# Performance work log

Measured on AMD Instinct MI355X. Metric: run time of the kernel, lower is better.

Reference implementation:

```python
import jax, jax.numpy as jnp
import numpy as np

N, F_IN, F_OUT = 8192, 512, 256

def setup_inputs() -> dict:
    key = jax.random.key(0)
    kx, kW, ka = jax.random.split(key, 3)
    x = jax.random.normal(kx, (N, F_IN), dtype=jnp.float32)
    adj = jnp.ones((N, N), dtype=jnp.float32)  # accepted but unused by the original forward
    # nn.Linear(in, out, bias=False) stores weight as [out, in]
    W = jax.random.normal(kW, (F_OUT, F_IN), dtype=jnp.float32) * 0.02
    # nn.Linear(2*out, 1, bias=False) -> attention vector of length 2*F_OUT
    a = jax.random.normal(ka, (2 * F_OUT,), dtype=jnp.float32) * 0.02
    return {"x": x, "adj": adj, "W": W, "a": a}

def reference(x, adj, W, a):
    # h = W(x): [N, F_OUT]
    h = x @ W.T
    # Original concatenates [h_i, h_j] for all pairs (O(N^2 * 2F) memory) and
    # applies linear a. Since a is linear, e_ij = a1.h_i + a2.h_j -> broadcast add.
    a_src, a_dst = a[:F_OUT], a[F_OUT:]
    e = (h @ a_src)[:, None] + (h @ a_dst)[None, :]  # [N, N]
    attention = jax.nn.softmax(e, axis=1)             # row-wise over neighbors j
    h_prime = attention @ h                           # [N, F_OUT]
    return h_prime
```

## Files before the change

### kernel.cpp

```cpp
#include <hip/hip_runtime.h>
#include <math.h>

#define NN 8192
#define FIN 512
#define FOUT 256
#define FBLK 512
#define NU 8


__global__ __launch_bounds__(256) void compute_g(const float* __restrict__ W,
                                                 const float* __restrict__ a_dst,
                                                 float* __restrict__ g,
                                                 float* __restrict__ u8,
                                                 float* __restrict__ S) {
    __shared__ float red[4][64];
    const int tid = threadIdx.x;

    const int zi = blockIdx.x * 256 + tid;
    ((float2*)u8)[zi] = make_float2(0.f, 0.f);
    if (zi == 0) *S = 0.f;

    const int kl = tid & 63;
    const int cp = tid >> 6;
    const int k = blockIdx.x * 64 + kl;
    float s = 0.f;
    #pragma unroll 8
    for (int c = cp * 64; c < cp * 64 + 64; ++c)
        s = fmaf(W[(size_t)c * FIN + k], a_dst[c], s);
    red[cp][kl] = s;
    __syncthreads();
    if (cp == 0) g[k] = red[0][kl] + red[1][kl] + red[2][kl] + red[3][kl];
}

__global__ __launch_bounds__(256) void fused_pass(const float* __restrict__ x,
                                                  const float* __restrict__ g,
                                                  float* __restrict__ u8,
                                                  float* __restrict__ S) {
    __shared__ float us[4][FIN];
    __shared__ float sred[4];
    const int tid = threadIdx.x;
    const int lane = tid & 63;
    const int wave = tid >> 6;
    const int r0 = blockIdx.x * 16;

    const float4* g4 = (const float4*)g;
    const float4 g0 = g4[lane], g1 = g4[lane + 64];

    float4 xa[4], xb[4];
    float w[4];
    #pragma unroll
    for (int rr = 0; rr < 4; ++rr) {
        const float4* xr = (const float4*)(x + (size_t)(r0 + wave * 4 + rr) * FIN);
        xa[rr] = xr[lane];
        xb[rr] = xr[lane + 64];
        float s = xa[rr].x * g0.x + xa[rr].y * g0.y + xa[rr].z * g0.z + xa[rr].w * g0.w
                + xb[rr].x * g1.x + xb[rr].y * g1.y + xb[rr].z * g1.z + xb[rr].w * g1.w;
        #pragma unroll
        for (int off = 32; off; off >>= 1) s += __shfl_xor(s, off);
        w[rr] = __expf(s);
    }
    if (lane == 0) sred[wave] = w[0] + w[1] + w[2] + w[3];

    float4 pa = make_float4(0.f, 0.f, 0.f, 0.f);
    float4 pb = make_float4(0.f, 0.f, 0.f, 0.f);
    #pragma unroll
    for (int rr = 0; rr < 4; ++rr) {
        pa.x = fmaf(w[rr], xa[rr].x, pa.x); pa.y = fmaf(w[rr], xa[rr].y, pa.y);
        pa.z = fmaf(w[rr], xa[rr].z, pa.z); pa.w = fmaf(w[rr], xa[rr].w, pa.w);
        pb.x = fmaf(w[rr], xb[rr].x, pb.x); pb.y = fmaf(w[rr], xb[rr].y, pb.y);
        pb.z = fmaf(w[rr], xb[rr].z, pb.z); pb.w = fmaf(w[rr], xb[rr].w, pb.w);
    }
    ((float4*)&us[wave][0])[lane] = pa;
    ((float4*)&us[wave][FOUT])[lane] = pb;
    __syncthreads();

    float* ub = u8 + (size_t)(blockIdx.x & (NU - 1)) * FIN;
    float v0 = us[0][tid] + us[1][tid] + us[2][tid] + us[3][tid];
    float v1 = us[0][tid + 256] + us[1][tid + 256] + us[2][tid + 256] + us[3][tid + 256];
    atomicAdd(&ub[tid], v0);
    atomicAdd(&ub[tid + 256], v1);
    if (tid == 0) atomicAdd(S, sred[0] + sred[1] + sred[2] + sred[3]);
}

__global__ __launch_bounds__(256) void compute_v(const float* __restrict__ W,
                                                 const float* __restrict__ u8,
                                                 const float* __restrict__ S,
                                                 float* __restrict__ vs) {
    __shared__ float us[FIN];
    const int tid = threadIdx.x;
    float a0 = 0.f, a1 = 0.f;
    #pragma unroll
    for (int i = 0; i < NU; ++i) {
        a0 += u8[(size_t)i * FIN + tid];
        a1 += u8[(size_t)i * FIN + tid + 256];
    }
    us[tid] = a0;
    us[tid + 256] = a1;
    __syncthreads();

    const int lane = tid & 63;
    const int wave = tid >> 6;
    const int c = blockIdx.x * 4 + wave;
    const float4* wr = (const float4*)(W + (size_t)c * FIN);
    const float4* uv = (const float4*)us;
    float4 w0 = wr[lane], w1 = wr[lane + 64];
    float4 u0 = uv[lane], u1 = uv[lane + 64];
    float s = w0.x * u0.x + w0.y * u0.y + w0.z * u0.z + w0.w * u0.w
            + w1.x * u1.x + w1.y * u1.y + w1.z * u1.z + w1.w * u1.w;
    #pragma unroll
    for (int off = 32; off; off >>= 1) s += __shfl_xor(s, off);
    if (lane == 0) vs[c] = s / *S;
}

__global__ __launch_bounds__(256) void broadcast_out(const float* __restrict__ vs,
                                                     float* __restrict__ out) {
    const int idx = blockIdx.x * 256 + threadIdx.x;
    float4 vv = ((const float4*)vs)[idx & 63];
    ((float4*)out)[idx] = vv;
}

extern "C" void kernel_launch(void* const* d_in, const int* in_sizes, int n_in,
                              void* d_out, int out_size, void* d_ws, size_t ws_size,
                              hipStream_t stream) {
    const float* x = (const float*)d_in[0];
    const float* W = (const float*)d_in[2];
    const float* a = (const float*)d_in[3];
    float* out = (float*)d_out;

    float* ws = (float*)d_ws;
    float* g  = ws;
    float* u8 = ws + 512;
    float* S  = ws + 512 + NU * FIN;
    float* vs = S + 16;

    compute_g<<<8, 256, 0, stream>>>(W, a + FOUT, g, u8, S);
    fused_pass<<<FBLK, 256, 0, stream>>>(x, g, u8, S);
    compute_v<<<FOUT / 4, 256, 0, stream>>>(W, u8, S, vs);
    broadcast_out<<<(NN * FOUT / 4) / 256, 256, 0, stream>>>(vs, out);
}
```

Before: 323.3 us.

## Fuse all GAT stages into one cooperative kernel with grid-wide syncs

Replaces the four separate launches with one cooperative kernel that uses grid syncs between stages: computing g, the weighted row reduction into u8 and S, the W·u projection, and the output broadcast. Each block now recomputes the full 256-output projection from W and writes its own 16 output rows directly. This removes per-launch overhead and inter-kernel gaps. In exchange it adds redundant reads of W across all blocks (strided per-thread row access) and the cost of grid barriers. The old four-kernel path remains as a fallback if the cooperative launch fails.

Measured after the change: 463.4 us. 43.3% more time.

```diff
diff --git a/kernel.cpp b/kernel.cpp
--- a/kernel.cpp
+++ b/kernel.cpp
@@ -1,12 +1,131 @@
 #include <hip/hip_runtime.h>
+#include <hip/hip_cooperative_groups.h>
 #include <math.h>
+
+namespace cg = cooperative_groups;
 
 #define NN 8192
 #define FIN 512
 #define FOUT 256
-#define FBLK 512
+#define GRID 512
 #define NU 8
 
+
+__global__ __launch_bounds__(256, 2) void gat_fused_all(
+    const float* __restrict__ x,
+    const float* __restrict__ W,
+    const float* __restrict__ a_dst,
+    float* __restrict__ out,
+    float* __restrict__ g,
+    float* __restrict__ u8,
+    float* __restrict__ S)
+{
+    cg::grid_group gg = cg::this_grid();
+
+    __shared__ float us[4][FIN];
+    __shared__ float sred[4];
+    __shared__ float vsh[FOUT];
+
+    const int tid  = threadIdx.x;
+    const int bid  = blockIdx.x;
+    const int lane = tid & 63;
+    const int wave = tid >> 6;
+    const int r0   = bid * 16;
+
+    if (bid < 8) {
+        const int zi = bid * 256 + tid;
+        ((float2*)u8)[zi] = make_float2(0.f, 0.f);
+        if (zi == 0) *S = 0.f;
+
+        const int k = bid * 64 + lane;
+        float s = 0.f;
+        #pragma unroll 8
+        for (int c = wave * 64; c < wave * 64 + 64; ++c)
+            s = fmaf(W[(size_t)c * FIN + k], a_dst[c], s);
+        us[wave][lane] = s;
+        __syncthreads();
+        if (wave == 0) g[k] = us[0][lane] + us[1][lane] + us[2][lane] + us[3][lane];
+    }
+    gg.sync();
+
+    const float4* g4 = (const float4*)g;
+    const float4 g0 = g4[lane], g1 = g4[lane + 64];
+
+    float4 xa[4], xb[4];
+    float w[4];
+    #pragma unroll
+    for (int rr = 0; rr < 4; ++rr) {
+        const float4* xr = (const float4*)(x + (size_t)(r0 + wave * 4 + rr) * FIN);
+        xa[rr] = xr[lane];
+        xb[rr] = xr[lane + 64];
+        float s = xa[rr].x * g0.x + xa[rr].y * g0.y + xa[rr].z * g0.z + xa[rr].w * g0.w
+                + xb[rr].x * g1.x + xb[rr].y * g1.y + xb[rr].z * g1.z + xb[rr].w * g1.w;
+        #pragma unroll
+        for (int off = 32; off; off >>= 1) s += __shfl_xor(s, off);
+        w[rr] = __expf(s);
+    }
+    if (lane == 0) sred[wave] = w[0] + w[1] + w[2] + w[3];
+
+    float4 pa = make_float4(0.f, 0.f, 0.f, 0.f);
+    float4 pb = make_float4(0.f, 0.f, 0.f, 0.f);
+    #pragma unroll
+    for (int rr = 0; rr < 4; ++rr) {
+        pa.x = fmaf(w[rr], xa[rr].x, pa.x); pa.y = fmaf(w[rr], xa[rr].y, pa.y);
+        pa.z = fmaf(w[rr], xa[rr].z, pa.z); pa.w = fmaf(w[rr], xa[rr].w, pa.w);
+        pb.x = fmaf(w[rr], xb[rr].x, pb.x); pb.y = fmaf(w[rr], xb[rr].y, pb.y);
+        pb.z = fmaf(w[rr], xb[rr].z, pb.z); pb.w = fmaf(w[rr], xb[rr].w, pb.w);
+    }
+    ((float4*)&us[wave][0])[lane]    = pa;
+    ((float4*)&us[wave][FOUT])[lane] = pb;
+    __syncthreads();
+
+    {
+        float* ub = u8 + (size_t)(bid & (NU - 1)) * FIN;
+        float v0 = us[0][tid]       + us[1][tid]       + us[2][tid]       + us[3][tid];
+        float v1 = us[0][tid + 256] + us[1][tid + 256] + us[2][tid + 256] + us[3][tid + 256];
+        atomicAdd(&ub[tid], v0);
+        atomicAdd(&ub[tid + 256], v1);
+        if (tid == 0) atomicAdd(S, sred[0] + sred[1] + sred[2] + sred[3]);
+    }
+    gg.sync();
+
+    {
+        float a0 = 0.f, a1 = 0.f;
+        #pragma unroll
+        for (int i = 0; i < NU; ++i) {
+            a0 += u8[(size_t)i * FIN + tid];
+            a1 += u8[(size_t)i * FIN + tid + 256];
+        }
+        us[0][tid]       = a0;
+        us[0][tid + 256] = a1;
+    }
+    __syncthreads();
+
+    {
+        const float rS = 1.f / (*S);
+        const float4* u4 = (const float4*)&us[0][0];
+        const float4* wr = (const float4*)(W + (size_t)tid * FIN);
+        float s = 0.f;
+        #pragma unroll 16
+        for (int i = 0; i < FIN / 4; ++i) {
+            const float4 wv = wr[i];
+            const float4 uv = u4[i];
+            s += wv.x * uv.x + wv.y * uv.y + wv.z * uv.z + wv.w * uv.w;
+        }
+        vsh[tid] = s * rS;
+    }
+    __syncthreads();
+
+    {
+        const float4* v4 = (const float4*)vsh;
+        float4* ob = (float4*)out + (size_t)r0 * (FOUT / 4);
+        #pragma unroll
+        for (int q = 0; q < 4; ++q) {
+            const int fi = q * 256 + tid;
+            ob[fi] = v4[fi & 63];
+        }
+    }
+}
 
 __global__ __launch_bounds__(256) void compute_g(const float* __restrict__ W,
                                                  const float* __restrict__ a_dst,
@@ -15,11 +134,9 @@
                                                  float* __restrict__ S) {
     __shared__ float red[4][64];
     const int tid = threadIdx.x;
-
     const int zi = blockIdx.x * 256 + tid;
     ((float2*)u8)[zi] = make_float2(0.f, 0.f);
     if (zi == 0) *S = 0.f;
-
     const int kl = tid & 63;
     const int cp = tid >> 6;
     const int k = blockIdx.x * 64 + kl;
@@ -42,10 +159,8 @@
     const int lane = tid & 63;
     const int wave = tid >> 6;
     const int r0 = blockIdx.x * 16;
-
     const float4* g4 = (const float4*)g;
     const float4 g0 = g4[lane], g1 = g4[lane + 64];
-
     float4 xa[4], xb[4];
     float w[4];
     #pragma unroll
@@ -60,7 +175,6 @@
         w[rr] = __expf(s);
     }
     if (lane == 0) sred[wave] = w[0] + w[1] + w[2] + w[3];
-
     float4 pa = make_float4(0.f, 0.f, 0.f, 0.f);
     float4 pb = make_float4(0.f, 0.f, 0.f, 0.f);
     #pragma unroll
@@ -73,7 +187,6 @@
     ((float4*)&us[wave][0])[lane] = pa;
     ((float4*)&us[wave][FOUT])[lane] = pb;
     __syncthreads();
-
     float* ub = u8 + (size_t)(blockIdx.x & (NU - 1)) * FIN;
     float v0 = us[0][tid] + us[1][tid] + us[2][tid] + us[3][tid];
     float v1 = us[0][tid + 256] + us[1][tid + 256] + us[2][tid + 256] + us[3][tid + 256];
@@ -97,7 +210,6 @@
     us[tid] = a0;
     us[tid + 256] = a1;
     __syncthreads();
-
     const int lane = tid & 63;
     const int wave = tid >> 6;
     const int c = blockIdx.x * 4 + wave;
@@ -125,6 +237,7 @@
     const float* x = (const float*)d_in[0];
     const float* W = (const float*)d_in[2];
     const float* a = (const float*)d_in[3];
+    const float* a_dst = a + FOUT;
     float* out = (float*)d_out;
 
     float* ws = (float*)d_ws;
@@ -133,8 +246,16 @@
     float* S  = ws + 512 + NU * FIN;
     float* vs = S + 16;
 
-    compute_g<<<8, 256, 0, stream>>>(W, a + FOUT, g, u8, S);
-    fused_pass<<<FBLK, 256, 0, stream>>>(x, g, u8, S);
-    compute_v<<<FOUT / 4, 256, 0, stream>>>(W, u8, S, vs);
-    broadcast_out<<<(NN * FOUT / 4) / 256, 256, 0, stream>>>(vs, out);
-}
+    void* args[] = {(void*)&x, (void*)&W, (void*)&a_dst, (void*)&out,
+                    (void*)&g, (void*)&u8, (void*)&S};
+    hipError_t err = hipLaunchCooperativeKernel(
+        reinterpret_cast<void*>(gat_fused_all), dim3(GRID), dim3(256),
+        args, 0, stream);
+
+    if (err != hipSuccess) {
+        compute_g<<<8, 256, 0, stream>>>(W, a_dst, g, u8, S);
+        fused_pass<<<GRID, 256, 0, stream>>>(x, g, u8, S);
+        compute_v<<<FOUT / 4, 256, 0, stream>>>(W, u8, S, vs);
+        broadcast_out<<<(NN * FOUT / 4) / 256, 256, 0, stream>>>(vs, out);
+    }
+}
```
